# Kernel tuning notes

Hardware: AMD Instinct MI355X
Metric: run time of the kernel (lower is better)

## Reference

```python
import jax, jax.numpy as jnp
import numpy as np

# model constants (from par)
DT = 0.05
TAU_M = 10.0
ALPHA = 1.0 - DT / TAU_M   # membrane leak factor
V_TH = 1.0                 # spike threshold
T, B, N = 500, 1024, 256


def setup_inputs() -> dict:
    key = jax.random.key(0)
    kx, kw = jax.random.split(key)
    x = jax.random.normal(kx, (T, B, N), dtype=jnp.float32)
    w = jax.random.normal(kw, (N,), dtype=jnp.float32) / np.sqrt(N).astype(np.float32)
    return {"x": x, "w": w}


def reference(x, w):
    """LIF neuron dynamics over T timesteps.

    Per step (matching NeuronClass_nn.__call__):
      v <- alpha * v + x_t @ w - v_th * stop_gradient(z)
      z <- 1[v - v_th > 0]
    Returns (v_seq, z_seq), each [T, B].
    """
    batch = x.shape[1]
    v0 = jnp.zeros((batch,), dtype=x.dtype)
    z0 = jnp.zeros((batch,), dtype=x.dtype)

    def step(carry, x_t):
        v, z = carry
        v = ALPHA * v + x_t @ w - V_TH * jax.lax.stop_gradient(z)
        z = (v - V_TH > 0).astype(v.dtype)
        return (v, z), (v, z)

    _, (v_seq, z_seq) = jax.lax.scan(step, (v0, z0), x)
    return v_seq, z_seq
```

## Files before the change

### kernel.cpp

```cpp
#include <hip/hip_runtime.h>

#define T_STEPS 500
#define BATCH   1024
#define NDIM    256
#define ALPHA_F 0.995f

__global__ __launch_bounds__(256) void lif_dot_kernel(
    const float* __restrict__ x, const float* __restrict__ w,
    float* __restrict__ s, int rows)
{
    int gtid = blockIdx.x * blockDim.x + threadIdx.x;
    int row  = gtid >> 6;
    int lane = threadIdx.x & 63;
    if (row >= rows) return;

    const float4 xv = *(const float4*)(x + (size_t)row * NDIM + lane * 4);
    const float4 wv = *(const float4*)(w + lane * 4);

    float p = xv.x * wv.x + xv.y * wv.y + xv.z * wv.z + xv.w * wv.w;

    p += __shfl_xor(p, 32, 64);
    p += __shfl_xor(p, 16, 64);
    p += __shfl_xor(p, 8, 64);
    p += __shfl_xor(p, 4, 64);
    p += __shfl_xor(p, 2, 64);
    p += __shfl_xor(p, 1, 64);

    if (lane == 0) s[row] = p;
}

__global__ __launch_bounds__(64) void lif_scan_kernel(
    float* __restrict__ vout, float* __restrict__ sz)
{
    int b = blockIdx.x * 64 + threadIdx.x;
    if (b >= BATCH) return;

    float v = 0.0f, z = 0.0f;

    float cur[4];
#pragma unroll
    for (int j = 0; j < 4; ++j) cur[j] = sz[(size_t)j * BATCH + b];

    for (int t0 = 0; t0 < T_STEPS; t0 += 4) {
        float nxt[4] = {0.f, 0.f, 0.f, 0.f};
        if (t0 + 4 < T_STEPS) {
#pragma unroll
            for (int j = 0; j < 4; ++j)
                nxt[j] = sz[(size_t)(t0 + 4 + j) * BATCH + b];
        }
#pragma unroll
        for (int j = 0; j < 4; ++j) {
            float sv = cur[j];
            v = (ALPHA_F * v + sv) - z;
            z = (v - 1.0f > 0.0f) ? 1.0f : 0.0f;
            vout[(size_t)(t0 + j) * BATCH + b] = v;
            sz  [(size_t)(t0 + j) * BATCH + b] = z;
        }
#pragma unroll
        for (int j = 0; j < 4; ++j) cur[j] = nxt[j];
    }
}

extern "C" void kernel_launch(void* const* d_in, const int* in_sizes, int n_in,
                              void* d_out, int out_size, void* d_ws, size_t ws_size,
                              hipStream_t stream)
{
    const float* x = (const float*)d_in[0];
    const float* w = (const float*)d_in[1];
    float* out = (float*)d_out;

    float* vout = out;
    float* sz   = out + (size_t)T_STEPS * BATCH;

    const int rows = T_STEPS * BATCH;
    const int waves_per_block = 4;
    const int blocks = (rows + waves_per_block - 1) / waves_per_block;

    lif_dot_kernel<<<blocks, 256, 0, stream>>>(x, w, sz, rows);
    lif_scan_kernel<<<BATCH / 64, 64, 0, stream>>>(vout, sz);
}
```

Before: 712.0 us.

## Fuse dot product and LIF scan into one per-batch wave kernel

Replaces the separate dot-product kernel and the serial scan kernel with one kernel. Each wavefront owns one batch element and walks all timesteps, computing the x_t·w reduction with shuffles and updating v/z in registers. Input rows are prefetched four steps ahead. This removes the intermediate buffer round trip, the second launch and the poorly parallel 16-block scan. In exchange the dot products for a batch element now run serially, and only 1024 waves are available to hide memory latency.

Result: slower. 730.7 us (+2.6%).

```diff
diff --git a/kernel.cpp b/kernel.cpp
--- a/kernel.cpp
+++ b/kernel.cpp
@@ -1,60 +1,53 @@
 #include <hip/hip_runtime.h>
+
 
 #define T_STEPS 500
 #define BATCH   1024
 #define NDIM    256
 #define ALPHA_F 0.995f
+#define TSTRIDE ((size_t)BATCH * NDIM)
 
-__global__ __launch_bounds__(256) void lif_dot_kernel(
+__global__ __launch_bounds__(256) void lif_fused_kernel(
     const float* __restrict__ x, const float* __restrict__ w,
-    float* __restrict__ s, int rows)
+    float* __restrict__ vout, float* __restrict__ zout)
 {
-    int gtid = blockIdx.x * blockDim.x + threadIdx.x;
-    int row  = gtid >> 6;
-    int lane = threadIdx.x & 63;
-    if (row >= rows) return;
+    const int wave = threadIdx.x >> 6;
+    const int lane = threadIdx.x & 63;
+    const int c    = blockIdx.x * 4 + wave;
 
-    const float4 xv = *(const float4*)(x + (size_t)row * NDIM + lane * 4);
     const float4 wv = *(const float4*)(w + lane * 4);
-
-    float p = xv.x * wv.x + xv.y * wv.y + xv.z * wv.z + xv.w * wv.w;
-
-    p += __shfl_xor(p, 32, 64);
-    p += __shfl_xor(p, 16, 64);
-    p += __shfl_xor(p, 8, 64);
-    p += __shfl_xor(p, 4, 64);
-    p += __shfl_xor(p, 2, 64);
-    p += __shfl_xor(p, 1, 64);
-
-    if (lane == 0) s[row] = p;
-}
-
-__global__ __launch_bounds__(64) void lif_scan_kernel(
-    float* __restrict__ vout, float* __restrict__ sz)
-{
-    int b = blockIdx.x * 64 + threadIdx.x;
-    if (b >= BATCH) return;
+    const float* xbase = x + (size_t)c * NDIM + lane * 4;
 
     float v = 0.0f, z = 0.0f;
 
-    float cur[4];
+    float4 cur[4], nxt[4];
 #pragma unroll
-    for (int j = 0; j < 4; ++j) cur[j] = sz[(size_t)j * BATCH + b];
+    for (int j = 0; j < 4; ++j)
+        cur[j] = *(const float4*)(xbase + (size_t)j * TSTRIDE);
 
     for (int t0 = 0; t0 < T_STEPS; t0 += 4) {
-        float nxt[4] = {0.f, 0.f, 0.f, 0.f};
-        if (t0 + 4 < T_STEPS) {
+        const int tp = (t0 + 4 < T_STEPS) ? (t0 + 4) : t0;
 #pragma unroll
-            for (int j = 0; j < 4; ++j)
-                nxt[j] = sz[(size_t)(t0 + 4 + j) * BATCH + b];
-        }
+        for (int j = 0; j < 4; ++j)
+            nxt[j] = *(const float4*)(xbase + (size_t)(tp + j) * TSTRIDE);
+
 #pragma unroll
         for (int j = 0; j < 4; ++j) {
-            float sv = cur[j];
-            v = (ALPHA_F * v + sv) - z;
+            float p = cur[j].x * wv.x + cur[j].y * wv.y
+                    + cur[j].z * wv.z + cur[j].w * wv.w;
+            p += __shfl_xor(p, 32, 64);
+            p += __shfl_xor(p, 16, 64);
+            p += __shfl_xor(p, 8, 64);
+            p += __shfl_xor(p, 4, 64);
+            p += __shfl_xor(p, 2, 64);
+            p += __shfl_xor(p, 1, 64);
+
+            v = ALPHA_F * v + p - z;
             z = (v - 1.0f > 0.0f) ? 1.0f : 0.0f;
-            vout[(size_t)(t0 + j) * BATCH + b] = v;
-            sz  [(size_t)(t0 + j) * BATCH + b] = z;
+
+            const size_t o = (size_t)(t0 + j) * BATCH + c;
+            if (lane == 0) vout[o] = v;
+            if (lane == 1) zout[o] = z;
         }
 #pragma unroll
         for (int j = 0; j < 4; ++j) cur[j] = nxt[j];
@@ -67,15 +60,9 @@
 {
     const float* x = (const float*)d_in[0];
     const float* w = (const float*)d_in[1];
-    float* out = (float*)d_out;
+    float* out  = (float*)d_out;
+    float* vout = out;
+    float* zout = out + (size_t)T_STEPS * BATCH;
 
-    float* vout = out;
-    float* sz   = out + (size_t)T_STEPS * BATCH;
-
-    const int rows = T_STEPS * BATCH;
-    const int waves_per_block = 4;
-    const int blocks = (rows + waves_per_block - 1) / waves_per_block;
-
-    lif_dot_kernel<<<blocks, 256, 0, stream>>>(x, w, sz, rows);
-    lif_scan_kernel<<<BATCH / 64, 64, 0, stream>>>(vout, sz);
+    lif_fused_kernel<<<BATCH / 4, 256, 0, stream>>>(x, w, vout, zout);
 }
```
